# Performance work log

Measured on AMD Instinct MI355X. Metric: run time of the kernel, lower is better.

## Reference

```python
import jax, jax.numpy as jnp
import numpy as np

N = 100000   # nodes
E = 1600000  # edges
G = 64       # graphs in batch
IN = 5
H = 2        # GAT heads
HID = 64
NCLS = 4


def setup_inputs() -> dict:
    key = jax.random.key(0)
    ks = jax.random.split(key, 16)
    rn = lambda k, s: (jax.random.normal(k, s, dtype=jnp.float32) * 0.1)
    f32 = jnp.float32
    return {
        "x": jax.random.normal(ks[0], (N, IN), dtype=f32),
        "edge_index": jax.random.randint(ks[1], (2, E), 0, N),
        "batch": jnp.sort(jax.random.randint(ks[2], (N,), 0, G)),
        # GATConv(5 -> 64, heads=2, concat=True)
        "gat_w": rn(ks[3], (IN, H * HID)),
        "att_src": rn(ks[4], (H, HID)),
        "att_dst": rn(ks[5], (H, HID)),
        "gat_b": jnp.zeros((H * HID,), f32),
        "bn1_g": jnp.ones((H * HID,), f32), "bn1_b": jnp.zeros((H * HID,), f32),
        # SAGEConv(128 -> 64): lin_l (aggregated, with bias) + lin_r (root, no bias)
        "sage_wl": rn(ks[6], (H * HID, HID)), "sage_bl": jnp.zeros((HID,), f32),
        "sage_wr": rn(ks[7], (H * HID, HID)),
        "bn2_g": jnp.ones((HID,), f32), "bn2_b": jnp.zeros((HID,), f32),
        # GCNConv(64 -> 64)
        "gcn_w": rn(ks[8], (HID, HID)), "gcn_b": jnp.zeros((HID,), f32),
        "bn3_g": jnp.ones((HID,), f32), "bn3_b": jnp.zeros((HID,), f32),
        # classifier MLP 128 -> 64 -> 4
        "w1": rn(ks[9], (2 * HID, HID)), "b1": jnp.zeros((HID,), f32),
        "w2": rn(ks[10], (HID, NCLS)), "b2": jnp.zeros((NCLS,), f32),
    }


def _bn(h, g, b):
    # BatchNorm in training-stats mode (dropout is treated as eval/identity)
    m = h.mean(0)
    v = h.var(0)
    return (h - m) * jax.lax.rsqrt(v + 1e-5) * g + b


def _forward(x, edge_index, batch, gat_w, att_src, att_dst, gat_b, bn1_g, bn1_b,
             sage_wl, sage_bl, sage_wr, bn2_g, bn2_b, gcn_w, gcn_b, bn3_g, bn3_b,
             w1, b1, w2, b2):
    src, dst = edge_index[0], edge_index[1]  # message flows src -> dst

    # ---- GATConv (heads=2, concat) ----
    xw = (x @ gat_w).reshape(-1, H, HID)                  # [N,H,C]
    a_src = (xw * att_src).sum(-1)                        # [N,H]
    a_dst = (xw * att_dst).sum(-1)                        # [N,H]
    e = jax.nn.leaky_relu(a_src[src] + a_dst[dst], 0.2)   # [E,H]
    e_max = jax.ops.segment_max(e, dst, num_segments=N)
    e_max = jnp.where(jnp.isfinite(e_max), e_max, 0.0)
    ex = jnp.exp(e - e_max[dst])
    denom = jax.ops.segment_sum(ex, dst, num_segments=N)
    alpha = ex / (denom[dst] + 1e-16)                     # segment softmax over incoming edges
    h = jax.ops.segment_sum(xw[src] * alpha[:, :, None], dst, num_segments=N)
    h = h.reshape(-1, H * HID) + gat_b
    h = jax.nn.elu(_bn(h, bn1_g, bn1_b))

    # ---- SAGEConv (mean aggregation) ----
    deg = jax.ops.segment_sum(jnp.ones((E,), h.dtype), dst, num_segments=N)
    agg = jax.ops.segment_sum(h[src], dst, num_segments=N) / jnp.maximum(deg, 1.0)[:, None]
    h = agg @ sage_wl + sage_bl + h @ sage_wr
    h = jax.nn.elu(_bn(h, bn2_g, bn2_b))

    # ---- GCNConv (symmetric norm, self loops) ----
    hw = h @ gcn_w
    deg_sl = deg + 1.0  # degree with self loop
    dinv = jax.lax.rsqrt(deg_sl)
    msg = hw[src] * (dinv[src] * dinv[dst])[:, None]
    h = jax.ops.segment_sum(msg, dst, num_segments=N) + hw * (dinv * dinv)[:, None] + gcn_b
    h = jax.nn.elu(_bn(h, bn3_g, bn3_b))

    # ---- global mean + max pool over graphs ----
    cnt = jax.ops.segment_sum(jnp.ones((h.shape[0],), h.dtype), batch, num_segments=G)
    pmean = jax.ops.segment_sum(h, batch, num_segments=G) / jnp.maximum(cnt, 1.0)[:, None]
    pmax = jax.ops.segment_max(h, batch, num_segments=G)
    pmax = jnp.where(jnp.isfinite(pmax), pmax, 0.0)
    z = jnp.concatenate([pmean, pmax], axis=1)            # [G, 2*HID]

    # ---- classifier ----
    z = jax.nn.relu(z @ w1 + b1)
    return z @ w2 + b2                                    # [G, NCLS]


def reference(x, edge_index, batch, gat_w, att_src, att_dst, gat_b, bn1_g, bn1_b,
              sage_wl, sage_bl, sage_wr, bn2_g, bn2_b, gcn_w, gcn_b, bn3_g, bn3_b,
              w1, b1, w2, b2):
    return _forward(x, edge_index, batch, gat_w, att_src, att_dst, gat_b, bn1_g, bn1_b,
                    sage_wl, sage_bl, sage_wr, bn2_g, bn2_b, gcn_w, gcn_b, bn3_g, bn3_b,
                    w1, b1, w2, b2)
```

## Files before the change

### kernel.cpp

```cpp
#include <hip/hip_runtime.h>
#include <hip/hip_bf16.h>
#include <math.h>

#define NN 100000
#define NE 1600000
#define NG 64
#define F_IN 5
#define F1 128
#define F2 64
#define NCLS 4
#define NCHUNK 250
#define CH_E 6400
#define NBUCK ((NN + 255) / 256)
#define CAPB 6144

typedef unsigned short ushort;
typedef __bf16 bf16x8 __attribute__((ext_vector_type(8)));
typedef float f32x4 __attribute__((ext_vector_type(4)));

__device__ __forceinline__ ushort f2bf(float f) {
    unsigned u = __float_as_uint(f);
    u = (u + 0x7fffu + ((u >> 16) & 1u)) >> 16;
    return (ushort)u;
}
__device__ __forceinline__ float bf2f(ushort h) {
    return __uint_as_float(((unsigned)h) << 16);
}
__device__ __forceinline__ unsigned pack2bf(float a, float b) {
    return (unsigned)f2bf(a) | ((unsigned)f2bf(b) << 16);
}
__device__ __forceinline__ float lo_bf(unsigned p) { return __uint_as_float(p << 16); }
__device__ __forceinline__ float hi_bf(unsigned p) { return __uint_as_float(p & 0xffff0000u); }

__device__ __forceinline__ unsigned enc_f(float f) {
    unsigned b = __float_as_uint(f);
    return (b & 0x80000000u) ? ~b : (b | 0x80000000u);
}
__device__ __forceinline__ float dec_f(unsigned k) {
    unsigned b = (k & 0x80000000u) ? (k ^ 0x80000000u) : ~k;
    return __uint_as_float(b);
}
#define ENC_NEG_INF 0x007FFFFFu

__global__ void k_fill_u32(unsigned* p, unsigned v, int n) {
    int i = blockIdx.x * blockDim.x + threadIdx.x;
    if (i < n) p[i] = v;
}

__global__ void k_packfrag_dual(const float* __restrict__ wl, const float* __restrict__ wr,
                                ushort* __restrict__ frag) {
    int idx = blockIdx.x * 256 + threadIdx.x;
    if (idx >= 4 * 8 * 64 * 8) return;
    int e = idx & 7;
    int lane = (idx >> 3) & 63;
    int ct = (idx >> 9) & 7;
    int ks = idx >> 12;
    int k = ks * 32 + (lane >> 4) * 8 + e;
    int n = ct * 16 + (lane & 15);
    float val = (n < 64) ? wl[k * 64 + n] : wr[k * 64 + (n - 64)];
    frag[idx] = f2bf(val);
}

__global__ void k_packfrag_gcn(const float* __restrict__ wm, ushort* __restrict__ frag) {
    int idx = blockIdx.x * 256 + threadIdx.x;
    if (idx >= 2 * 4 * 64 * 8) return;
    int e = idx & 7;
    int lane = (idx >> 3) & 63;
    int ct = (idx >> 9) & 3;
    int ks = idx >> 11;
    int k = ks * 32 + (lane >> 4) * 8 + e;
    int n = ct * 16 + (lane & 15);
    frag[idx] = f2bf(wm[k * 64 + n]);
}

__global__ void k_hist(const int* __restrict__ ei, int* __restrict__ ghist) {
    __shared__ int lh[NBUCK];
    int c = blockIdx.x, t = threadIdx.x;
    for (int b = t; b < NBUCK; b += 256) lh[b] = 0;
    __syncthreads();
    int e0 = c * CH_E;
#pragma unroll
    for (int i = 0; i < CH_E / 256; i++) {
        int d = ei[NE + e0 + t + i * 256];
        atomicAdd(&lh[d >> 8], 1);
    }
    __syncthreads();
    for (int b = t; b < NBUCK; b += 256) ghist[c * NBUCK + b] = lh[b];
}

__global__ void k_bchunkscan(int* __restrict__ ghist, int* __restrict__ bbase,
                             int* __restrict__ rowptr) {
    __shared__ int sh[512];
    int b = threadIdx.x;
    int tot = 0;
    if (b < NBUCK)
        for (int c = 0; c < NCHUNK; c++) tot += ghist[c * NBUCK + b];
    sh[b] = tot;
    __syncthreads();
    for (int off = 1; off < 512; off <<= 1) {
        int v = (b >= off) ? sh[b - off] : 0;
        __syncthreads();
        sh[b] += v;
        __syncthreads();
    }
    int base = sh[b] - tot;
    if (b <= NBUCK) bbase[b] = (b < NBUCK) ? base : NE;
    if (b == 0) rowptr[NN] = NE;
    int run = base;
    if (b < NBUCK)
        for (int c = 0; c < NCHUNK; c++) {
            int h = ghist[c * NBUCK + b];
            ghist[c * NBUCK + b] = run;
            run += h;
        }
}

__global__ void k_scatter2(const int* __restrict__ ei, const int* __restrict__ ghist,
                           unsigned* __restrict__ staged) {
    __shared__ int lcur[NBUCK];
    int c = blockIdx.x, t = threadIdx.x;
    for (int b = t; b < NBUCK; b += 256) lcur[b] = ghist[c * NBUCK + b];
    __syncthreads();
    int e0 = c * CH_E;
#pragma unroll
    for (int i = 0; i < CH_E / 256; i++) {
        int e = e0 + t + i * 256;
        int s = ei[e];
        int d = ei[NE + e];
        int pos = atomicAdd(&lcur[d >> 8], 1);
        staged[pos] = (((unsigned)(d & 255)) << 17) | (unsigned)s;
    }
}

__global__ void k_bucket_sort(const unsigned* __restrict__ staged, const int* __restrict__ bbase,
                              int* __restrict__ rowptr, int* __restrict__ csr_src) {
    __shared__ unsigned ein[CAPB];
    __shared__ unsigned sout[CAPB];
    __shared__ int lhist[256];
    __shared__ int lps[256];
    int b = blockIdx.x, t = threadIdx.x;
    int n0 = b * 256;
    int g0 = bbase[b];
    int m = bbase[b + 1] - g0;
    lhist[t] = 0;
    __syncthreads();
    if (m <= CAPB) {
        for (int i = t; i < m; i += 256) {
            unsigned u = staged[g0 + i];
            ein[i] = u;
            atomicAdd(&lhist[u >> 17], 1);
        }
        __syncthreads();
        lps[t] = lhist[t];
        __syncthreads();
        for (int off = 1; off < 256; off <<= 1) {
            int v = (t >= off) ? lps[t - off] : 0;
            __syncthreads();
            lps[t] += v;
            __syncthreads();
        }
        int excl = lps[t] - lhist[t];
        if (n0 + t < NN) rowptr[n0 + t] = g0 + excl;
        __syncthreads();
        lhist[t] = excl;
        __syncthreads();
        for (int i = t; i < m; i += 256) {
            unsigned u = ein[i];
            int pos = atomicAdd(&lhist[u >> 17], 1);
            sout[pos] = u & 0x1FFFFu;
        }
        __syncthreads();
        for (int i = t; i < m; i += 256) csr_src[g0 + i] = (int)sout[i];
    } else {
        for (int i = t; i < m; i += 256) {
            unsigned u = staged[g0 + i];
            atomicAdd(&lhist[u >> 17], 1);
        }
        __syncthreads();
        lps[t] = lhist[t];
        __syncthreads();
        for (int off = 1; off < 256; off <<= 1) {
            int v = (t >= off) ? lps[t - off] : 0;
            __syncthreads();
            lps[t] += v;
            __syncthreads();
        }
        int excl = lps[t] - lhist[t];
        if (n0 + t < NN) rowptr[n0 + t] = g0 + excl;
        __syncthreads();
        lhist[t] = excl;
        __syncthreads();
        for (int i = t; i < m; i += 256) {
            unsigned u = staged[g0 + i];
            int pos = atomicAdd(&lhist[u >> 17], 1);
            csr_src[g0 + pos] = (int)(u & 0x1FFFFu);
        }
    }
}

__global__ void k_xw(const float* __restrict__ x, const float* __restrict__ gw,
                     const float* __restrict__ aw_src, const float* __restrict__ aw_dst,
                     unsigned* __restrict__ xw32, float* __restrict__ a_src,
                     float* __restrict__ a_dst) {
    __shared__ float w[F_IN * F1];
    int t = threadIdx.x;
    for (int i = t; i < F_IN * F1; i += 256) w[i] = gw[i];
    int wv = t >> 6, lane = t & 63;
    int f0 = 2 * lane, f1 = 2 * lane + 1;
    float as0 = aw_src[f0], as1 = aw_src[f1];
    float ad0 = aw_dst[f0], ad1 = aw_dst[f1];
    __syncthreads();
    int nbase = blockIdx.x * 64;
    for (int it = 0; it < 16; it++) {
        int n = nbase + it * 4 + wv;
        if (n >= NN) break;
        float xs[F_IN];
#pragma unroll
        for (int j = 0; j < F_IN; j++) xs[j] = x[n * F_IN + j];
        float acc0 = 0.f, acc1 = 0.f;
#pragma unroll
        for (int j = 0; j < F_IN; j++) {
            acc0 += xs[j] * w[j * F1 + f0];
            acc1 += xs[j] * w[j * F1 + f1];
        }
        xw32[(size_t)n * 64 + lane] = pack2bf(acc0, acc1);
        float p = acc0 * as0 + acc1 * as1;
        float q = acc0 * ad0 + acc1 * ad1;
#pragma unroll
        for (int off = 1; off < 32; off <<= 1) {
            p += __shfl_xor(p, off);
            q += __shfl_xor(q, off);
        }
        if (lane == 0)  { a_src[n * 2 + 0] = p; a_dst[n * 2 + 0] = q; }
        if (lane == 32) { a_src[n * 2 + 1] = p; a_dst[n * 2 + 1] = q; }
    }
}

__global__ void k_gat_gather(const int* __restrict__ rowptr, const int* __restrict__ csr_src,
                             const float* __restrict__ a_src, const float* __restrict__ a_dst,
                             const unsigned* __restrict__ xw32, float* __restrict__ h1) {
    int n = blockIdx.x * 4 + (threadIdx.x >> 6);
    int lane = threadIdx.x & 63;
    if (n >= NN) return;
    int j0 = rowptr[n], j1 = rowptr[n + 1];
    int deg = j1 - j0;
    float ad0 = a_dst[n * 2 + 0], ad1 = a_dst[n * 2 + 1];
    float acc0 = 0.f, acc1 = 0.f;
    bool lo = (lane < 32);
    if (deg <= 64) {
        int sl = 0;
        float l0 = -INFINITY, l1 = -INFINITY;
        if (lane < deg) {
            sl = csr_src[j0 + lane];
            l0 = a_src[sl * 2 + 0] + ad0;
            l1 = a_src[sl * 2 + 1] + ad1;
            l0 = l0 > 0.f ? l0 : 0.2f * l0;
            l1 = l1 > 0.f ? l1 : 0.2f * l1;
        }
        float m0 = l0, m1 = l1;
#pragma unroll
        for (int off = 32; off > 0; off >>= 1) {
            m0 = fmaxf(m0, __shfl_xor(m0, off));
            m1 = fmaxf(m1, __shfl_xor(m1, off));
        }
        float e0 = 0.f, e1 = 0.f;
        if (lane < deg) { e0 = expf(l0 - m0); e1 = expf(l1 - m1); }
        float s0 = e0, s1 = e1;
#pragma unroll
        for (int off = 32; off > 0; off >>= 1) {
            s0 += __shfl_xor(s0, off);
            s1 += __shfl_xor(s1, off);
        }
        unsigned al = pack2bf(e0 / (s0 + 1e-16f), e1 / (s1 + 1e-16f));
        int e = 0;
        for (; e + 4 <= deg; e += 4) {
            int s0i = __shfl(sl, e + 0), s1i = __shfl(sl, e + 1),
                s2i = __shfl(sl, e + 2), s3i = __shfl(sl, e + 3);
            unsigned b0 = __shfl(al, e + 0), b1 = __shfl(al, e + 1),
                     b2 = __shfl(al, e + 2), b3 = __shfl(al, e + 3);
            unsigned p0 = xw32[(size_t)s0i * 64 + lane];
            unsigned p1 = xw32[(size_t)s1i * 64 + lane];
            unsigned p2 = xw32[(size_t)s2i * 64 + lane];
            unsigned p3 = xw32[(size_t)s3i * 64 + lane];
            float w0 = lo ? lo_bf(b0) : hi_bf(b0);
            float w1 = lo ? lo_bf(b1) : hi_bf(b1);
            float w2 = lo ? lo_bf(b2) : hi_bf(b2);
            float w3 = lo ? lo_bf(b3) : hi_bf(b3);
            acc0 = fmaf(lo_bf(p0), w0, acc0); acc1 = fmaf(hi_bf(p0), w0, acc1);
            acc0 = fmaf(lo_bf(p1), w1, acc0); acc1 = fmaf(hi_bf(p1), w1, acc1);
            acc0 = fmaf(lo_bf(p2), w2, acc0); acc1 = fmaf(hi_bf(p2), w2, acc1);
            acc0 = fmaf(lo_bf(p3), w3, acc0); acc1 = fmaf(hi_bf(p3), w3, acc1);
        }
        for (; e < deg; e++) {
            int s = __shfl(sl, e); unsigned b = __shfl(al, e);
            unsigned p = xw32[(size_t)s * 64 + lane];
            float w = lo ? lo_bf(b) : hi_bf(b);
            acc0 = fmaf(lo_bf(p), w, acc0);
            acc1 = fmaf(hi_bf(p), w, acc1);
        }
    } else {
        float m0 = -INFINITY, m1 = -INFINITY, s0 = 0.f, s1 = 0.f;
        for (int base = j0; base < j1; base += 64) {
            int myj = base + lane;
            float l0 = -INFINITY, l1 = -INFINITY;
            if (myj < j1) {
                int s = csr_src[myj];
                l0 = a_src[s * 2 + 0] + ad0;
                l1 = a_src[s * 2 + 1] + ad1;
                l0 = l0 > 0.f ? l0 : 0.2f * l0;
                l1 = l1 > 0.f ? l1 : 0.2f * l1;
            }
            float cm0 = l0, cm1 = l1;
#pragma unroll
            for (int off = 32; off > 0; off >>= 1) {
                cm0 = fmaxf(cm0, __shfl_xor(cm0, off));
                cm1 = fmaxf(cm1, __shfl_xor(cm1, off));
            }
            float nm0 = fmaxf(m0, cm0), nm1 = fmaxf(m1, cm1);
            float ce0 = (myj < j1) ? expf(l0 - nm0) : 0.f;
            float ce1 = (myj < j1) ? expf(l1 - nm1) : 0.f;
            float cs0 = ce0, cs1 = ce1;
#pragma unroll
            for (int off = 32; off > 0; off >>= 1) {
                cs0 += __shfl_xor(cs0, off);
                cs1 += __shfl_xor(cs1, off);
            }
            s0 = s0 * expf(m0 - nm0) + cs0;
            s1 = s1 * expf(m1 - nm1) + cs1;
            m0 = nm0; m1 = nm1;
        }
        float r0 = 1.0f / (s0 + 1e-16f), r1 = 1.0f / (s1 + 1e-16f);
        for (int base = j0; base < j1; base += 64) {
            int cnt = min(64, j1 - base);
            int myj = base + lane;
            int sl = 0; unsigned al = 0;
            if (myj < j1) {
                sl = csr_src[myj];
                float l0 = a_src[sl * 2 + 0] + ad0;
                float l1 = a_src[sl * 2 + 1] + ad1;
                l0 = l0 > 0.f ? l0 : 0.2f * l0;
                l1 = l1 > 0.f ? l1 : 0.2f * l1;
                al = pack2bf(expf(l0 - m0) * r0, expf(l1 - m1) * r1);
            }
            int e = 0;
            for (; e + 4 <= cnt; e += 4) {
                int s0i = __shfl(sl, e + 0), s1i = __shfl(sl, e + 1),
                    s2i = __shfl(sl, e + 2), s3i = __shfl(sl, e + 3);
                unsigned b0 = __shfl(al, e + 0), b1 = __shfl(al, e + 1),
                         b2 = __shfl(al, e + 2), b3 = __shfl(al, e + 3);
                unsigned p0 = xw32[(size_t)s0i * 64 + lane];
                unsigned p1 = xw32[(size_t)s1i * 64 + lane];
                unsigned p2 = xw32[(size_t)s2i * 64 + lane];
                unsigned p3 = xw32[(size_t)s3i * 64 + lane];
                float w0 = lo ? lo_bf(b0) : hi_bf(b0);
                float w1 = lo ? lo_bf(b1) : hi_bf(b1);
                float w2 = lo ? lo_bf(b2) : hi_bf(b2);
                float w3 = lo ? lo_bf(b3) : hi_bf(b3);
                acc0 = fmaf(lo_bf(p0), w0, acc0); acc1 = fmaf(hi_bf(p0), w0, acc1);
                acc0 = fmaf(lo_bf(p1), w1, acc0); acc1 = fmaf(hi_bf(p1), w1, acc1);
                acc0 = fmaf(lo_bf(p2), w2, acc0); acc1 = fmaf(hi_bf(p2), w2, acc1);
                acc0 = fmaf(lo_bf(p3), w3, acc0); acc1 = fmaf(hi_bf(p3), w3, acc1);
            }
            for (; e < cnt; e++) {
                int s = __shfl(sl, e); unsigned b = __shfl(al, e);
                unsigned p = xw32[(size_t)s * 64 + lane];
                float w = lo ? lo_bf(b) : hi_bf(b);
                acc0 = fmaf(lo_bf(p), w, acc0);
                acc1 = fmaf(hi_bf(p), w, acc1);
            }
        }
    }
    float2 o; o.x = acc0; o.y = acc1;
    *(float2*)&h1[(size_t)n * F1 + 2 * lane] = o;
}

__global__ void k_bn_stats(const float* __restrict__ h, int nfeat, float* __restrict__ sums) {
    __shared__ float sh[512];
    int t = threadIdx.x;
    int f = t & (nfeat - 1);
    int rg = t / nfeat;
    int R = 256 / nfeat;
    int rows = (NN + gridDim.x - 1) / gridDim.x;
    int rbase = blockIdx.x * rows;
    int r1 = min(NN, rbase + rows);
    float s = 0.f, ss = 0.f;
    for (int r = rbase + rg; r < r1; r += R) {
        float v = h[(size_t)r * nfeat + f];
        s += v; ss += v * v;
    }
    sh[t] = s; sh[256 + t] = ss;
    __syncthreads();
    if (rg == 0) {
        for (int g = 1; g < R; g++) {
            s += sh[g * nfeat + f];
            ss += sh[256 + g * nfeat + f];
        }
        atomicAdd(&sums[f], s);
        atomicAdd(&sums[nfeat + f], ss);
    }
}

__global__ void k_bn_apply_bf(const float* __restrict__ h, const float* __restrict__ sums,
                              const float* __restrict__ g, const float* __restrict__ b,
                              int nfeat, int total, ushort* __restrict__ hb) {
    int i = blockIdx.x * blockDim.x + threadIdx.x;
    if (i >= total) return;
    int f = i & (nfeat - 1);
    float m = sums[f] * (1.0f / NN);
    float var = sums[nfeat + f] * (1.0f / NN) - m * m;
    float v = (h[i] - m) * rsqrtf(var + 1e-5f) * g[f] + b[f];
    hb[i] = f2bf(v > 0.f ? v : expm1f(v));
}

__global__ void k_sage_dualgemm(const ushort* __restrict__ h1b, const ushort* __restrict__ fragd,
                                ushort* __restrict__ u_bf, float* __restrict__ v) {
    __shared__ uint4 sfrag[2048];
    int t = threadIdx.x;
    const uint4* f4 = (const uint4*)fragd;
    for (int i = t; i < 2048; i += 256) sfrag[i] = f4[i];
    __syncthreads();
    int w = t >> 6, lane = t & 63;
    int row0 = blockIdx.x * 64 + w * 16;
    int arow = row0 + (lane & 15);
    if (arow >= NN) arow = NN - 1;
    f32x4 acc[8];
#pragma unroll
    for (int c = 0; c < 8; c++) acc[c] = (f32x4){0.f, 0.f, 0.f, 0.f};
#pragma unroll
    for (int ks = 0; ks < 4; ks++) {
        union { uint4 u; bf16x8 f; } ua;
        ua.u = *(const uint4*)&h1b[(size_t)arow * F1 + ks * 32 + (lane >> 4) * 8];
#pragma unroll
        for (int ct = 0; ct < 8; ct++) {
            union { uint4 u; bf16x8 f; } ub;
            ub.u = sfrag[(ks * 8 + ct) * 64 + lane];
            acc[ct] = __builtin_amdgcn_mfma_f32_16x16x32_bf16(ua.f, ub.f, acc[ct], 0, 0, 0);
        }
    }
    int mrow0 = row0 + (lane >> 4) * 4;
    int n = lane & 15;
#pragma unroll
    for (int reg = 0; reg < 4; reg++) {
        int r = mrow0 + reg;
        if (r >= NN) continue;
#pragma unroll
        for (int ct = 0; ct < 4; ct++)
            u_bf[(size_t)r * F2 + ct * 16 + n] = f2bf(acc[ct][reg]);
#pragma unroll
        for (int ct = 4; ct < 8; ct++)
            v[(size_t)r * F2 + (ct - 4) * 16 + n] = acc[ct][reg];
    }
}

__global__ void k_sage_gather2(const int* __restrict__ rowptr, const int* __restrict__ csr_src,
                               const ushort* __restrict__ u_bf, const float* __restrict__ v,
                               const float* __restrict__ bl, float* __restrict__ h2) {
    int n = blockIdx.x * 4 + (threadIdx.x >> 6);
    int lane = threadIdx.x & 63;
    if (n >= NN) return;
    int j0 = rowptr[n], j1 = rowptr[n + 1];
    float a = 0.f;
    for (int base = j0; base < j1; base += 64) {
        int cnt = min(64, j1 - base);
        int myj = base + lane;
        int sl = (myj < j1) ? csr_src[myj] : 0;
        int e = 0;
        for (; e + 4 <= cnt; e += 4) {
            int s0 = __shfl(sl, e + 0), s1 = __shfl(sl, e + 1),
                s2 = __shfl(sl, e + 2), s3 = __shfl(sl, e + 3);
            float t0 = bf2f(u_bf[(size_t)s0 * F2 + lane]);
            float t1 = bf2f(u_bf[(size_t)s1 * F2 + lane]);
            float t2 = bf2f(u_bf[(size_t)s2 * F2 + lane]);
            float t3 = bf2f(u_bf[(size_t)s3 * F2 + lane]);
            a += (t0 + t1) + (t2 + t3);
        }
        for (; e < cnt; e++) {
            int s = __shfl(sl, e);
            a += bf2f(u_bf[(size_t)s * F2 + lane]);
        }
    }
    float inv = 1.0f / fmaxf((float)(j1 - j0), 1.0f);
    h2[(size_t)n * F2 + lane] = a * inv + v[(size_t)n * F2 + lane] + bl[lane];
}

__global__ void k_dinv(const int* __restrict__ rowptr, float* __restrict__ dinv) {
    int i = blockIdx.x * blockDim.x + threadIdx.x;
    if (i < NN) dinv[i] = rsqrtf((float)(rowptr[i + 1] - rowptr[i]) + 1.0f);
}

__global__ void k_gcn_gemm(const ushort* __restrict__ h2b, const ushort* __restrict__ fragg,
                           const float* __restrict__ dinv, ushort* __restrict__ hwd_bf) {
    __shared__ uint4 sfrag[512];
    int t = threadIdx.x;
    const uint4* f4 = (const uint4*)fragg;
    for (int i = t; i < 512; i += 256) sfrag[i] = f4[i];
    __syncthreads();
    int w = t >> 6, lane = t & 63;
    int row0 = blockIdx.x * 64 + w * 16;
    int arow = row0 + (lane & 15);
    if (arow >= NN) arow = NN - 1;
    f32x4 acc[4];
#pragma unroll
    for (int c = 0; c < 4; c++) acc[c] = (f32x4){0.f, 0.f, 0.f, 0.f};
#pragma unroll
    for (int ks = 0; ks < 2; ks++) {
        union { uint4 u; bf16x8 f; } ua;
        ua.u = *(const uint4*)&h2b[(size_t)arow * F2 + ks * 32 + (lane >> 4) * 8];
#pragma unroll
        for (int ct = 0; ct < 4; ct++) {
            union { uint4 u; bf16x8 f; } ub;
            ub.u = sfrag[(ks * 4 + ct) * 64 + lane];
            acc[ct] = __builtin_amdgcn_mfma_f32_16x16x32_bf16(ua.f, ub.f, acc[ct], 0, 0, 0);
        }
    }
    int mrow0 = row0 + (lane >> 4) * 4;
    int n = lane & 15;
#pragma unroll
    for (int reg = 0; reg < 4; reg++) {
        int r = mrow0 + reg;
        if (r >= NN) continue;
        float d = dinv[r];
#pragma unroll
        for (int ct = 0; ct < 4; ct++)
            hwd_bf[(size_t)r * F2 + ct * 16 + n] = f2bf(acc[ct][reg] * d);
    }
}

__global__ void k_gcn_gather(const int* __restrict__ rowptr, const int* __restrict__ csr_src,
                             const ushort* __restrict__ hwd_bf, const float* __restrict__ dinv,
                             const float* __restrict__ gb, float* __restrict__ h3) {
    int n = blockIdx.x * 4 + (threadIdx.x >> 6);
    int lane = threadIdx.x & 63;
    if (n >= NN) return;
    int j0 = rowptr[n], j1 = rowptr[n + 1];
    float acc = 0.f;
    for (int base = j0; base < j1; base += 64) {
        int cnt = min(64, j1 - base);
        int myj = base + lane;
        int sl = (myj < j1) ? csr_src[myj] : 0;
        int e = 0;
        for (; e + 4 <= cnt; e += 4) {
            int s0 = __shfl(sl, e + 0), s1 = __shfl(sl, e + 1),
                s2 = __shfl(sl, e + 2), s3 = __shfl(sl, e + 3);
            float t0 = bf2f(hwd_bf[(size_t)s0 * F2 + lane]);
            float t1 = bf2f(hwd_bf[(size_t)s1 * F2 + lane]);
            float t2 = bf2f(hwd_bf[(size_t)s2 * F2 + lane]);
            float t3 = bf2f(hwd_bf[(size_t)s3 * F2 + lane]);
            acc += (t0 + t1) + (t2 + t3);
        }
        for (; e < cnt; e++) {
            int s = __shfl(sl, e);
            acc += bf2f(hwd_bf[(size_t)s * F2 + lane]);
        }
    }
    float di = dinv[n];
    acc += bf2f(hwd_bf[(size_t)n * F2 + lane]);
    h3[(size_t)n * F2 + lane] = acc * di + gb[lane];
}

__global__ void k_bn3_pool(const float* __restrict__ h3raw, const float* __restrict__ sums,
                           const float* __restrict__ g3, const float* __restrict__ b3,
                           const int* __restrict__ batch, float* __restrict__ psum,
                           unsigned* __restrict__ pmax, float* __restrict__ cnt) {
    int w = threadIdx.x >> 6;
    int lane = threadIdx.x & 63;
    int chunk = blockIdx.x * 4 + w;
    int nchunks = gridDim.x * 4;
    int rows = (NN + nchunks - 1) / nchunks;
    int r0 = chunk * rows;
    int r1 = min(NN, r0 + rows);
    if (r0 >= r1) return;
    float m = sums[lane] * (1.0f / NN);
    float var = sums[F2 + lane] * (1.0f / NN) - m * m;
    float sc = rsqrtf(var + 1e-5f) * g3[lane];
    float bb = b3[lane];
    int curg = batch[r0];
    float ls = 0.f, lm = -INFINITY;
    int run = 0;
    for (int r = r0; r < r1; r++) {
        int gg = batch[r];
        if (gg != curg) {
            atomicAdd(&psum[curg * F2 + lane], ls);
            atomicMax(&pmax[curg * F2 + lane], enc_f(lm));
            if (lane == 0) atomicAdd(&cnt[curg], (float)run);
            curg = gg; ls = 0.f; lm = -INFINITY; run = 0;
        }
        float v = (h3raw[(size_t)r * F2 + lane] - m) * sc + bb;
        v = v > 0.f ? v : expm1f(v);
        ls += v; lm = fmaxf(lm, v); run++;
    }
    atomicAdd(&psum[curg * F2 + lane], ls);
    atomicMax(&pmax[curg * F2 + lane], enc_f(lm));
    if (lane == 0) atomicAdd(&cnt[curg], (float)run);
}

__global__ void k_cls(const float* __restrict__ psum, const unsigned* __restrict__ pmax,
                      const float* __restrict__ cnt, const float* __restrict__ w1,
                      const float* __restrict__ b1, const float* __restrict__ w2,
                      const float* __restrict__ b2, float* __restrict__ out) {
    int g = blockIdx.x;
    int j = threadIdx.x;
    __shared__ float z[2 * F2];
    __shared__ float hid[F2];
    float c = fmaxf(cnt[g], 1.0f);
    z[j] = psum[g * F2 + j] / c;
    float mv = dec_f(pmax[g * F2 + j]);
    z[F2 + j] = isfinite(mv) ? mv : 0.f;
    __syncthreads();
    float acc = b1[j];
#pragma unroll 8
    for (int k = 0; k < 2 * F2; k++) acc += z[k] * w1[k * F2 + j];
    hid[j] = fmaxf(acc, 0.f);
    __syncthreads();
    if (j < NCLS) {
        float o = b2[j];
#pragma unroll 8
        for (int k = 0; k < F2; k++) o += hid[k] * w2[k * NCLS + j];
        out[g * NCLS + j] = o;
    }
}

extern "C" void kernel_launch(void* const* d_in, const int* in_sizes, int n_in,
                              void* d_out, int out_size, void* d_ws, size_t ws_size,
                              hipStream_t stream) {
    const float* x       = (const float*)d_in[0];
    const int*   ei      = (const int*)d_in[1];
    const int*   batch   = (const int*)d_in[2];
    const float* gat_w   = (const float*)d_in[3];
    const float* att_src = (const float*)d_in[4];
    const float* att_dst = (const float*)d_in[5];
    const float* bn1_g   = (const float*)d_in[7];
    const float* bn1_b   = (const float*)d_in[8];
    const float* sage_wl = (const float*)d_in[9];
    const float* sage_bl = (const float*)d_in[10];
    const float* sage_wr = (const float*)d_in[11];
    const float* bn2_g   = (const float*)d_in[12];
    const float* bn2_b   = (const float*)d_in[13];
    const float* gcn_w   = (const float*)d_in[14];
    const float* gcn_b   = (const float*)d_in[15];
    const float* bn3_g   = (const float*)d_in[16];
    const float* bn3_b   = (const float*)d_in[17];
    const float* w1      = (const float*)d_in[18];
    const float* b1      = (const float*)d_in[19];
    const float* w2      = (const float*)d_in[20];
    const float* b2      = (const float*)d_in[21];
    float* out = (float*)d_out;

    float* ws = (float*)d_ws;
    size_t o_A    = 0;
    size_t o_h1   = o_A   + (size_t)NN * F1;
    size_t o_h2   = o_h1  + (size_t)NN * F1;
    size_t o_csr  = o_h2  + (size_t)NN * F2;
    size_t o_rp   = o_csr + (size_t)NE;
    size_t o_bb   = o_rp  + (size_t)(NN + 4);
    size_t o_asrc = o_bb  + 400;
    size_t o_adst = o_asrc + (size_t)NN * 2;
    size_t o_dinv = o_adst + (size_t)NN * 2;
    size_t o_sums = o_dinv + (size_t)NN;
    size_t o_frd  = o_sums + 256;
    size_t o_frg  = o_frd  + 8192;
    size_t o_psum = o_frg  + 2048;
    size_t o_pmax = o_psum + (size_t)NG * F2;
    size_t o_cnt  = o_pmax + (size_t)NG * F2;

    float* A    = ws + o_A;
    float* h1   = ws + o_h1;
    float* h2   = ws + o_h2;
    int* csr_src = (int*)(ws + o_csr);
    int* rowptr  = (int*)(ws + o_rp);
    int* bbase   = (int*)(ws + o_bb);
    float* asr  = ws + o_asrc;
    float* ads  = ws + o_adst;
    float* dinv = ws + o_dinv;
    float* sums = ws + o_sums;
    ushort* fragd = (ushort*)(ws + o_frd);
    ushort* fragg = (ushort*)(ws + o_frg);
    float* psum = ws + o_psum;
    unsigned* pmax = (unsigned*)(ws + o_pmax);
    float* cnt  = ws + o_cnt;

    unsigned* staged = (unsigned*)A;
    int*    ghist  = (int*)(A + 2 * 1024 * 1024);
    unsigned* xw32 = (unsigned*)A;
    ushort* u_bf   = (ushort*)A;
    float*  vmat   = A + (size_t)NN * F2 / 2;
    ushort* hwd_bf = (ushort*)A;
    float*  h3     = A + (size_t)NN * F2 / 2;
    ushort* h1b    = (ushort*)h2;
    ushort* h2b    = (ushort*)h1;

    k_hist<<<NCHUNK, 256, 0, stream>>>(ei, ghist);
    k_bchunkscan<<<1, 512, 0, stream>>>(ghist, bbase, rowptr);
    k_scatter2<<<NCHUNK, 256, 0, stream>>>(ei, ghist, staged);
    k_bucket_sort<<<NBUCK, 256, 0, stream>>>(staged, bbase, rowptr, csr_src);

    k_xw<<<(NN + 63) / 64, 256, 0, stream>>>(x, gat_w, att_src, att_dst, xw32, asr, ads);
    k_gat_gather<<<(NN + 3) / 4, 256, 0, stream>>>(rowptr, csr_src, asr, ads, xw32, h1);
    hipMemsetAsync(sums, 0, sizeof(float) * 256, stream);
    k_bn_stats<<<1024, 256, 0, stream>>>(h1, F1, sums);
    k_bn_apply_bf<<<(NN * F1 + 255) / 256, 256, 0, stream>>>(h1, sums, bn1_g, bn1_b,
                                                             F1, NN * F1, h1b);

    k_packfrag_dual<<<(16384 + 255) / 256, 256, 0, stream>>>(sage_wl, sage_wr, fragd);
    k_sage_dualgemm<<<(NN + 63) / 64, 256, 0, stream>>>(h1b, fragd, u_bf, vmat);
    k_sage_gather2<<<(NN + 3) / 4, 256, 0, stream>>>(rowptr, csr_src, u_bf, vmat, sage_bl, h2);
    hipMemsetAsync(sums, 0, sizeof(float) * 256, stream);
    k_bn_stats<<<1024, 256, 0, stream>>>(h2, F2, sums);
    k_bn_apply_bf<<<(NN * F2 + 255) / 256, 256, 0, stream>>>(h2, sums, bn2_g, bn2_b,
                                                             F2, NN * F2, h2b);

    k_dinv<<<(NN + 255) / 256, 256, 0, stream>>>(rowptr, dinv);
    k_packfrag_gcn<<<(4096 + 255) / 256, 256, 0, stream>>>(gcn_w, fragg);
    k_gcn_gemm<<<(NN + 63) / 64, 256, 0, stream>>>(h2b, fragg, dinv, hwd_bf);
    k_gcn_gather<<<(NN + 3) / 4, 256, 0, stream>>>(rowptr, csr_src, hwd_bf, dinv, gcn_b, h3);
    hipMemsetAsync(sums, 0, sizeof(float) * 256, stream);
    k_bn_stats<<<1024, 256, 0, stream>>>(h3, F2, sums);

    hipMemsetAsync(psum, 0, sizeof(float) * NG * F2, stream);
    hipMemsetAsync(cnt, 0, sizeof(float) * NG, stream);
    k_fill_u32<<<(NG * F2 + 255) / 256, 256, 0, stream>>>(pmax, ENC_NEG_INF, NG * F2);
    k_bn3_pool<<<1024, 256, 0, stream>>>(h3, sums, bn3_g, bn3_b, batch, psum, pmax, cnt);
    k_cls<<<NG, F2, 0, stream>>>(psum, pmax, cnt, w1, b1, w2, b2, out);
}
```

Baseline: 494.2 us.

## Store intermediate activations in bf16, parallelize bucket scan, fold dinv into sort

The gather kernels now write their pre-BatchNorm activations (h1, h2, h3) as bf16 instead of fp32, and the BN stats, apply and pool kernels read bf16. This halves the bytes written and read for these intermediates. The single-block chunk scan becomes a per-bucket parallel scan followed by a small prefix kernel. The dinv computation is moved into the bucket sort using its local histogram, and the memsets are batched at the start. The cost is extra bf16 rounding of pre-normalization activations, which adds some precision error.

Result: faster. 474.9 us (-3.9%).

```diff
diff --git a/kernel.cpp b/kernel.cpp
--- a/kernel.cpp
+++ b/kernel.cpp
@@ -88,38 +88,44 @@
     for (int b = t; b < NBUCK; b += 256) ghist[c * NBUCK + b] = lh[b];
 }
 
-__global__ void k_bchunkscan(int* __restrict__ ghist, int* __restrict__ bbase,
-                             int* __restrict__ rowptr) {
+__global__ void k_bscan(int* __restrict__ ghist, int* __restrict__ btot) {
+    __shared__ int sh[256];
+    int b = blockIdx.x, t = threadIdx.x;
+    int v = (t < NCHUNK) ? ghist[t * NBUCK + b] : 0;
+    sh[t] = v;
+    __syncthreads();
+    for (int off = 1; off < 256; off <<= 1) {
+        int u = (t >= off) ? sh[t - off] : 0;
+        __syncthreads();
+        sh[t] += u;
+        __syncthreads();
+    }
+    if (t < NCHUNK) ghist[t * NBUCK + b] = sh[t] - v;
+    if (t == 255) btot[b] = sh[255];
+}
+
+__global__ void k_bprefix(const int* __restrict__ btot, int* __restrict__ bbase,
+                          int* __restrict__ rowptr) {
     __shared__ int sh[512];
-    int b = threadIdx.x;
-    int tot = 0;
-    if (b < NBUCK)
-        for (int c = 0; c < NCHUNK; c++) tot += ghist[c * NBUCK + b];
-    sh[b] = tot;
+    int t = threadIdx.x;
+    int v = (t < NBUCK) ? btot[t] : 0;
+    sh[t] = v;
     __syncthreads();
     for (int off = 1; off < 512; off <<= 1) {
-        int v = (b >= off) ? sh[b - off] : 0;
-        __syncthreads();
-        sh[b] += v;
-        __syncthreads();
-    }
-    int base = sh[b] - tot;
-    if (b <= NBUCK) bbase[b] = (b < NBUCK) ? base : NE;
-    if (b == 0) rowptr[NN] = NE;
-    int run = base;
-    if (b < NBUCK)
-        for (int c = 0; c < NCHUNK; c++) {
-            int h = ghist[c * NBUCK + b];
-            ghist[c * NBUCK + b] = run;
-            run += h;
-        }
+        int u = (t >= off) ? sh[t - off] : 0;
+        __syncthreads();
+        sh[t] += u;
+        __syncthreads();
+    }
+    if (t < NBUCK) bbase[t] = sh[t] - v;
+    if (t == 0) { bbase[NBUCK] = NE; rowptr[NN] = NE; }
 }
 
 __global__ void k_scatter2(const int* __restrict__ ei, const int* __restrict__ ghist,
-                           unsigned* __restrict__ staged) {
+                           const int* __restrict__ bbase, unsigned* __restrict__ staged) {
     __shared__ int lcur[NBUCK];
     int c = blockIdx.x, t = threadIdx.x;
-    for (int b = t; b < NBUCK; b += 256) lcur[b] = ghist[c * NBUCK + b];
+    for (int b = t; b < NBUCK; b += 256) lcur[b] = ghist[c * NBUCK + b] + bbase[b];
     __syncthreads();
     int e0 = c * CH_E;
 #pragma unroll
@@ -133,7 +139,8 @@
 }
 
 __global__ void k_bucket_sort(const unsigned* __restrict__ staged, const int* __restrict__ bbase,
-                              int* __restrict__ rowptr, int* __restrict__ csr_src) {
+                              int* __restrict__ rowptr, int* __restrict__ csr_src,
+                              float* __restrict__ dinv) {
     __shared__ unsigned ein[CAPB];
     __shared__ unsigned sout[CAPB];
     __shared__ int lhist[256];
@@ -151,6 +158,7 @@
             atomicAdd(&lhist[u >> 17], 1);
         }
         __syncthreads();
+        if (n0 + t < NN) dinv[n0 + t] = rsqrtf((float)lhist[t] + 1.0f);
         lps[t] = lhist[t];
         __syncthreads();
         for (int off = 1; off < 256; off <<= 1) {
@@ -177,6 +185,7 @@
             atomicAdd(&lhist[u >> 17], 1);
         }
         __syncthreads();
+        if (n0 + t < NN) dinv[n0 + t] = rsqrtf((float)lhist[t] + 1.0f);
         lps[t] = lhist[t];
         __syncthreads();
         for (int off = 1; off < 256; off <<= 1) {
@@ -238,7 +247,7 @@
 
 __global__ void k_gat_gather(const int* __restrict__ rowptr, const int* __restrict__ csr_src,
                              const float* __restrict__ a_src, const float* __restrict__ a_dst,
-                             const unsigned* __restrict__ xw32, float* __restrict__ h1) {
+                             const unsigned* __restrict__ xw32, unsigned* __restrict__ h1p) {
     int n = blockIdx.x * 4 + (threadIdx.x >> 6);
     int lane = threadIdx.x & 63;
     if (n >= NN) return;
@@ -370,11 +379,10 @@
             }
         }
     }
-    float2 o; o.x = acc0; o.y = acc1;
-    *(float2*)&h1[(size_t)n * F1 + 2 * lane] = o;
-}
-
-__global__ void k_bn_stats(const float* __restrict__ h, int nfeat, float* __restrict__ sums) {
+    h1p[(size_t)n * 64 + lane] = pack2bf(acc0, acc1);
+}
+
+__global__ void k_bn_stats_bf(const ushort* __restrict__ h, int nfeat, float* __restrict__ sums) {
     __shared__ float sh[512];
     int t = threadIdx.x;
     int f = t & (nfeat - 1);
@@ -385,7 +393,7 @@
     int r1 = min(NN, rbase + rows);
     float s = 0.f, ss = 0.f;
     for (int r = rbase + rg; r < r1; r += R) {
-        float v = h[(size_t)r * nfeat + f];
+        float v = bf2f(h[(size_t)r * nfeat + f]);
         s += v; ss += v * v;
     }
     sh[t] = s; sh[256 + t] = ss;
@@ -400,7 +408,7 @@
     }
 }
 
-__global__ void k_bn_apply_bf(const float* __restrict__ h, const float* __restrict__ sums,
+__global__ void k_bn_apply_bf(const ushort* __restrict__ h, const float* __restrict__ sums,
                               const float* __restrict__ g, const float* __restrict__ b,
                               int nfeat, int total, ushort* __restrict__ hb) {
     int i = blockIdx.x * blockDim.x + threadIdx.x;
@@ -408,7 +416,7 @@
     int f = i & (nfeat - 1);
     float m = sums[f] * (1.0f / NN);
     float var = sums[nfeat + f] * (1.0f / NN) - m * m;
-    float v = (h[i] - m) * rsqrtf(var + 1e-5f) * g[f] + b[f];
+    float v = (bf2f(h[i]) - m) * rsqrtf(var + 1e-5f) * g[f] + b[f];
     hb[i] = f2bf(v > 0.f ? v : expm1f(v));
 }
 
@@ -454,7 +462,7 @@
 
 __global__ void k_sage_gather2(const int* __restrict__ rowptr, const int* __restrict__ csr_src,
                                const ushort* __restrict__ u_bf, const float* __restrict__ v,
-                               const float* __restrict__ bl, float* __restrict__ h2) {
+                               const float* __restrict__ bl, ushort* __restrict__ h2bf) {
     int n = blockIdx.x * 4 + (threadIdx.x >> 6);
     int lane = threadIdx.x & 63;
     if (n >= NN) return;
@@ -480,12 +488,7 @@
         }
     }
     float inv = 1.0f / fmaxf((float)(j1 - j0), 1.0f);
-    h2[(size_t)n * F2 + lane] = a * inv + v[(size_t)n * F2 + lane] + bl[lane];
-}
-
-__global__ void k_dinv(const int* __restrict__ rowptr, float* __restrict__ dinv) {
-    int i = blockIdx.x * blockDim.x + threadIdx.x;
-    if (i < NN) dinv[i] = rsqrtf((float)(rowptr[i + 1] - rowptr[i]) + 1.0f);
+    h2bf[(size_t)n * F2 + lane] = f2bf(a * inv + v[(size_t)n * F2 + lane] + bl[lane]);
 }
 
 __global__ void k_gcn_gemm(const ushort* __restrict__ h2b, const ushort* __restrict__ fragg,
@@ -528,7 +531,7 @@
 
 __global__ void k_gcn_gather(const int* __restrict__ rowptr, const int* __restrict__ csr_src,
                              const ushort* __restrict__ hwd_bf, const float* __restrict__ dinv,
-                             const float* __restrict__ gb, float* __restrict__ h3) {
+                             const float* __restrict__ gb, ushort* __restrict__ h3bf) {
     int n = blockIdx.x * 4 + (threadIdx.x >> 6);
     int lane = threadIdx.x & 63;
     if (n >= NN) return;
@@ -555,10 +558,10 @@
     }
     float di = dinv[n];
     acc += bf2f(hwd_bf[(size_t)n * F2 + lane]);
-    h3[(size_t)n * F2 + lane] = acc * di + gb[lane];
-}
-
-__global__ void k_bn3_pool(const float* __restrict__ h3raw, const float* __restrict__ sums,
+    h3bf[(size_t)n * F2 + lane] = f2bf(acc * di + gb[lane]);
+}
+
+__global__ void k_bn3_pool(const ushort* __restrict__ h3bf, const float* __restrict__ sums,
                            const float* __restrict__ g3, const float* __restrict__ b3,
                            const int* __restrict__ batch, float* __restrict__ psum,
                            unsigned* __restrict__ pmax, float* __restrict__ cnt) {
@@ -585,7 +588,7 @@
             if (lane == 0) atomicAdd(&cnt[curg], (float)run);
             curg = gg; ls = 0.f; lm = -INFINITY; run = 0;
         }
-        float v = (h3raw[(size_t)r * F2 + lane] - m) * sc + bb;
+        float v = (bf2f(h3bf[(size_t)r * F2 + lane]) - m) * sc + bb;
         v = v > 0.f ? v : expm1f(v);
         ls += v; lm = fmaxf(lm, v); run++;
     }
@@ -653,31 +656,35 @@
     size_t o_csr  = o_h2  + (size_t)NN * F2;
     size_t o_rp   = o_csr + (size_t)NE;
     size_t o_bb   = o_rp  + (size_t)(NN + 4);
-    size_t o_asrc = o_bb  + 400;
+    size_t o_bt   = o_bb  + 400;
+    size_t o_asrc = o_bt  + 400;
     size_t o_adst = o_asrc + (size_t)NN * 2;
     size_t o_dinv = o_adst + (size_t)NN * 2;
     size_t o_sums = o_dinv + (size_t)NN;
-    size_t o_frd  = o_sums + 256;
+    size_t o_frd  = o_sums + 768;
     size_t o_frg  = o_frd  + 8192;
     size_t o_psum = o_frg  + 2048;
-    size_t o_pmax = o_psum + (size_t)NG * F2;
-    size_t o_cnt  = o_pmax + (size_t)NG * F2;
+    size_t o_cnt  = o_psum + (size_t)NG * F2;
+    size_t o_pmax = o_cnt  + (size_t)NG;
 
     float* A    = ws + o_A;
-    float* h1   = ws + o_h1;
-    float* h2   = ws + o_h2;
+    float* h1r  = ws + o_h1;
+    float* h2r  = ws + o_h2;
     int* csr_src = (int*)(ws + o_csr);
     int* rowptr  = (int*)(ws + o_rp);
     int* bbase   = (int*)(ws + o_bb);
+    int* btot    = (int*)(ws + o_bt);
     float* asr  = ws + o_asrc;
     float* ads  = ws + o_adst;
     float* dinv = ws + o_dinv;
-    float* sums = ws + o_sums;
+    float* sums1 = ws + o_sums;
+    float* sums2 = sums1 + 256;
+    float* sums3 = sums2 + 256;
     ushort* fragd = (ushort*)(ws + o_frd);
     ushort* fragg = (ushort*)(ws + o_frg);
     float* psum = ws + o_psum;
+    float* cnt  = ws + o_cnt;
     unsigned* pmax = (unsigned*)(ws + o_pmax);
-    float* cnt  = ws + o_cnt;
 
     unsigned* staged = (unsigned*)A;
     int*    ghist  = (int*)(A + 2 * 1024 * 1024);
@@ -685,40 +692,41 @@
     ushort* u_bf   = (ushort*)A;
     float*  vmat   = A + (size_t)NN * F2 / 2;
     ushort* hwd_bf = (ushort*)A;
-    float*  h3     = A + (size_t)NN * F2 / 2;
-    ushort* h1b    = (ushort*)h2;
-    ushort* h2b    = (ushort*)h1;
+    ushort* h3bf   = (ushort*)(A + (size_t)NN * F2 / 2);
+    unsigned* h1p  = (unsigned*)h1r;
+    ushort* h1bf   = (ushort*)h1r;
+    ushort* h1b    = (ushort*)h2r;
+    ushort* h2bf   = (ushort*)h2r;
+    ushort* h2b    = (ushort*)h1r;
+
+    hipMemsetAsync(sums1, 0, sizeof(float) * 768, stream);
+    hipMemsetAsync(psum, 0, sizeof(float) * (NG * F2 + NG), stream);
+    k_fill_u32<<<(NG * F2 + 255) / 256, 256, 0, stream>>>(pmax, ENC_NEG_INF, NG * F2);
 
     k_hist<<<NCHUNK, 256, 0, stream>>>(ei, ghist);
-    k_bchunkscan<<<1, 512, 0, stream>>>(ghist, bbase, rowptr);
-    k_scatter2<<<NCHUNK, 256, 0, stream>>>(ei, ghist, staged);
-    k_bucket_sort<<<NBUCK, 256, 0, stream>>>(staged, bbase, rowptr, csr_src);
+    k_bscan<<<NBUCK, 256, 0, stream>>>(ghist, btot);
+    k_bprefix<<<1, 512, 0, stream>>>(btot, bbase, rowptr);
+    k_scatter2<<<NCHUNK, 256, 0, stream>>>(ei, ghist, bbase, staged);
+    k_bucket_sort<<<NBUCK, 256, 0, stream>>>(staged, bbase, rowptr, csr_src, dinv);
 
     k_xw<<<(NN + 63) / 64, 256, 0, stream>>>(x, gat_w, att_src, att_dst, xw32, asr, ads);
-    k_gat_gather<<<(NN + 3) / 4, 256, 0, stream>>>(rowptr, csr_src, asr, ads, xw32, h1);
-    hipMemsetAsync(sums, 0, sizeof(float) * 256, stream);
-    k_bn_stats<<<1024, 256, 0, stream>>>(h1, F1, sums);
-    k_bn_apply_bf<<<(NN * F1 + 255) / 256, 256, 0, stream>>>(h1, sums, bn1_g, bn1_b,
+    k_gat_gather<<<(NN + 3) / 4, 256, 0, stream>>>(rowptr, csr_src, asr, ads, xw32, h1p);
+    k_bn_stats_bf<<<1024, 256, 0, stream>>>(h1bf, F1, sums1);
+    k_bn_apply_bf<<<(NN * F1 + 255) / 256, 256, 0, stream>>>(h1bf, sums1, bn1_g, bn1_b,
                                                              F1, NN * F1, h1b);
 
     k_packfrag_dual<<<(16384 + 255) / 256, 256, 0, stream>>>(sage_wl, sage_wr, fragd);
     k_sage_dualgemm<<<(NN + 63) / 64, 256, 0, stream>>>(h1b, fragd, u_bf, vmat);
-    k_sage_gather2<<<(NN + 3) / 4, 256, 0, stream>>>(rowptr, csr_src, u_bf, vmat, sage_bl, h2);
-    hipMemsetAsync(sums, 0, sizeof(float) * 256, stream);
-    k_bn_stats<<<1024, 256, 0, stream>>>(h2, F2, sums);
-    k_bn_apply_bf<<<(NN * F2 + 255) / 256, 256, 0, stream>>>(h2, sums, bn2_g, bn2_b,
+    k_sage_gather2<<<(NN + 3) / 4, 256, 0, stream>>>(rowptr, csr_src, u_bf, vmat, sage_bl, h2bf);
+    k_bn_stats_bf<<<1024, 256, 0, stream>>>(h2bf, F2, sums2);
+    k_bn_apply_bf<<<(NN * F2 + 255) / 256, 256, 0, stream>>>(h2bf, sums2, bn2_g, bn2_b,
                                                              F2, NN * F2, h2b);
 
-    k_dinv<<<(NN + 255) / 256, 256, 0, stream>>>(rowptr, dinv);
     k_packfrag_gcn<<<(4096 + 255) / 256, 256, 0, stream>>>(gcn_w, fragg);
     k_gcn_gemm<<<(NN + 63) / 64, 256, 0, stream>>>(h2b, fragg, dinv, hwd_bf);
-    k_gcn_gather<<<(NN + 3) / 4, 256, 0, stream>>>(rowptr, csr_src, hwd_bf, dinv, gcn_b, h3);
-    hipMemsetAsync(sums, 0, sizeof(float) * 256, stream);
-    k_bn_stats<<<1024, 256, 0, stream>>>(h3, F2, sums);
-
-    hipMemsetAsync(psum, 0, sizeof(float) * NG * F2, stream);
-    hipMemsetAsync(cnt, 0, sizeof(float) * NG, stream);
-    k_fill_u32<<<(NG * F2 + 255) / 256, 256, 0, stream>>>(pmax, ENC_NEG_INF, NG * F2);
-    k_bn3_pool<<<1024, 256, 0, stream>>>(h3, sums, bn3_g, bn3_b, batch, psum, pmax, cnt);
+    k_gcn_gather<<<(NN + 3) / 4, 256, 0, stream>>>(rowptr, csr_src, hwd_bf, dinv, gcn_b, h3bf);
+    k_bn_stats_bf<<<1024, 256, 0, stream>>>(h3bf, F2, sums3);
+
+    k_bn3_pool<<<1024, 256, 0, stream>>>(h3bf, sums3, bn3_g, bn3_b, batch, psum, pmax, cnt);
     k_cls<<<NG, F2, 0, stream>>>(psum, pmax, cnt, w1, b1, w2, b2, out);
 }
```
